# Optimization experiments

Measured on AMD Instinct MI355X. Metric: run time of the kernel, lower is better.

The kernel has to match this reference:

```python
import jax, jax.numpy as jnp
import numpy as np

INPUT_DIM = 1024
MEMORY_DIM = 512
MEMORY_SIZE = 4096
TOPK = 8


def setup_inputs() -> dict:
    key = jax.random.key(0)
    ks = jax.random.split(key, 7)
    query = jax.random.normal(ks[0], (8, 4096, INPUT_DIM), dtype=jnp.float32)
    memory_keys = jax.random.normal(ks[1], (MEMORY_SIZE, MEMORY_DIM), dtype=jnp.float32)
    memory_values = jax.random.normal(ks[2], (MEMORY_SIZE, MEMORY_DIM), dtype=jnp.float32)
    # nn.Linear-style init (uniform +-1/sqrt(fan_in))
    wq = jax.random.uniform(ks[3], (INPUT_DIM, MEMORY_DIM), jnp.float32, -1.0, 1.0) / np.sqrt(INPUT_DIM)
    bq = jax.random.uniform(ks[4], (MEMORY_DIM,), jnp.float32, -1.0, 1.0) / np.sqrt(INPUT_DIM)
    wo = jax.random.uniform(ks[5], (MEMORY_DIM, INPUT_DIM), jnp.float32, -1.0, 1.0) / np.sqrt(MEMORY_DIM)
    bo = jax.random.uniform(ks[6], (INPUT_DIM,), jnp.float32, -1.0, 1.0) / np.sqrt(MEMORY_DIM)
    return {"query": query, "memory_keys": memory_keys, "memory_values": memory_values,
            "wq": wq, "bq": bq, "wo": wo, "bo": bo}


def reference(query, memory_keys, memory_values, wq, bq, wo, bo):
    B, S, D = query.shape
    # Query projection: [B,S,M]
    q = jnp.einsum('bsd,dm->bsm', query, wq) + bq
    # Scores vs memory keys: [B,S,memory_size] (no expand needed)
    scores = jnp.einsum('bsm,km->bsk', q, memory_keys)
    # Top-k selection + softmax over selected scores
    topk_w, topk_idx = jax.lax.top_k(scores, TOPK)           # [B,S,K]
    topk_w = jax.nn.softmax(topk_w, axis=-1)
    # Gather selected memory values: [B,S,K,M]
    top_vals = memory_values[topk_idx]
    mem_out = jnp.einsum('bskm,bsk->bsm', top_vals, topk_w)  # weighted sum
    out = jnp.einsum('bsm,md->bsd', mem_out, wo) + bo
    return out + query
```

## Files before the change

kernel.cpp:

```cpp
#include <hip/hip_runtime.h>
#include <cstdint>

typedef _Float16 f16;
typedef uint32_t u32;
typedef f16 f16x2 __attribute__((ext_vector_type(2)));
typedef f16 f16x8 __attribute__((ext_vector_type(8)));
typedef float f32x4 __attribute__((ext_vector_type(4)));
typedef float f32x16 __attribute__((ext_vector_type(16)));

#define NROWS 32768
#define D_IN 1024
#define M_DIM 512
#define NKEYS 4096
#define KTOP 8

__device__ __forceinline__ u32 umax32(u32 a, u32 b) { return a > b ? a : b; }
__device__ __forceinline__ u32 umin32(u32 a, u32 b) { return a < b ? a : b; }

__device__ __forceinline__ void gload_lds16(const void* src, void* dst) {
  __builtin_amdgcn_global_load_lds(
      (const __attribute__((address_space(1))) uint32_t*)src,
      (__attribute__((address_space(3))) uint32_t*)dst, 16, 0, 0);
}

__global__ void prep_kernel(const float* __restrict__ keys, const float* __restrict__ values,
                            const float* __restrict__ wq, const float* __restrict__ wo,
                            f16* __restrict__ keys_h, f16* __restrict__ values_h,
                            f16* __restrict__ wqT, f16* __restrict__ woT) {
  const int b = blockIdx.x, t = threadIdx.x;
  if (b < 2048) {
    const float* src = (b < 1024) ? keys : values;
    f16* dst = (b < 1024) ? keys_h : values_h;
    const int bb = b & 1023;
    const size_t base = (size_t)bb * 2048 + (size_t)t * 8;
    f32x4 a = *(const f32x4*)(src + base);
    f32x4 c2 = *(const f32x4*)(src + base + 4);
    f16x8 o;
    o[0] = (f16)a[0]; o[1] = (f16)a[1]; o[2] = (f16)a[2]; o[3] = (f16)a[3];
    o[4] = (f16)c2[0]; o[5] = (f16)c2[1]; o[6] = (f16)c2[2]; o[7] = (f16)c2[3];
    *(f16x8*)(dst + base) = o;
  } else if (b < 4096) {
    const int o = (b - 2048) * 256 + t;
    const int m = o >> 10, d = o & 1023;
    wqT[o] = (f16)wq[d * 512 + m];
  } else {
    const int o = (b - 4096) * 256 + t;
    const int od = o >> 9, mm = o & 511;
    woT[o] = (f16)wo[mm * 1024 + od];
  }
}

__global__ __launch_bounds__(256, 2) void qproj_kernel(
    const float* __restrict__ query, const f16* __restrict__ wqT,
    const float* __restrict__ bq, f16* __restrict__ q_out) {
  __shared__ f16 Atile[32 * 1024];
  const int tid = threadIdx.x;
  const int wave = tid >> 6, lane = tid & 63;
  const int g = lane >> 4, c = lane & 15;
  const int rowbase = blockIdx.x * 64 + wave * 16;
  const int row = rowbase + c;

  f16x8 Breg[32];
  {
    const float* qrow = query + (size_t)row * D_IN;
#pragma unroll
    for (int kk = 0; kk < 32; ++kk) {
      f32x4 lo = *(const f32x4*)(qrow + kk * 32 + g * 8);
      f32x4 hi = *(const f32x4*)(qrow + kk * 32 + g * 8 + 4);
      f16x8 v;
      v[0] = (f16)lo[0]; v[1] = (f16)lo[1]; v[2] = (f16)lo[2]; v[3] = (f16)lo[3];
      v[4] = (f16)hi[0]; v[5] = (f16)hi[1]; v[6] = (f16)hi[2]; v[7] = (f16)hi[3];
      Breg[kk] = v;
    }
  }

  for (int mt = 0; mt < 16; ++mt) {
    __syncthreads();
#pragma unroll
    for (int i2 = 0; i2 < 8; ++i2) {
      const int kr = wave * 8 + i2;
#pragma unroll
      for (int hb = 0; hb < 2; ++hb) {
        const u32 slot = (u32)(hb * 1024 + lane * 16);
        const u32 kb = slot ^ (u32)((kr & 7) << 4);
        const char* src = (const char*)(wqT + (size_t)(mt * 32 + kr) * D_IN) + kb;
        gload_lds16(src, (char*)Atile + kr * 2048 + hb * 1024);
      }
    }
    asm volatile("s_waitcnt vmcnt(0)" ::: "memory");
    __syncthreads();

    f32x4 acc0 = {0.f, 0.f, 0.f, 0.f};
    f32x4 acc1 = {0.f, 0.f, 0.f, 0.f};
#pragma unroll
    for (int kk = 0; kk < 32; ++kk) {
      const u32 base = (u32)(kk * 64 + g * 16);
      {
        const int ml = c;
        const u32 off = (u32)(ml * 2048) + (base ^ (u32)((ml & 7) << 4));
        f16x8 a = *(const f16x8*)((const char*)Atile + off);
        acc0 = __builtin_amdgcn_mfma_f32_16x16x32_f16(a, Breg[kk], acc0, 0, 0, 0);
      }
      {
        const int ml = 16 + c;
        const u32 off = (u32)(ml * 2048) + (base ^ (u32)((ml & 7) << 4));
        f16x8 a = *(const f16x8*)((const char*)Atile + off);
        acc1 = __builtin_amdgcn_mfma_f32_16x16x32_f16(a, Breg[kk], acc1, 0, 0, 0);
      }
    }

    f32x4 bq0 = *(const f32x4*)(bq + mt * 32 + g * 4);
    f32x4 bq1 = *(const f32x4*)(bq + mt * 32 + 16 + g * 4);
    f16* qp = q_out + (size_t)row * M_DIM + mt * 32 + g * 4;
    f16x2 p;
    p[0] = (f16)(acc0[0] + bq0[0]); p[1] = (f16)(acc0[1] + bq0[1]); *(f16x2*)(qp + 0) = p;
    p[0] = (f16)(acc0[2] + bq0[2]); p[1] = (f16)(acc0[3] + bq0[3]); *(f16x2*)(qp + 2) = p;
    p[0] = (f16)(acc1[0] + bq1[0]); p[1] = (f16)(acc1[1] + bq1[1]); *(f16x2*)(qp + 16) = p;
    p[0] = (f16)(acc1[2] + bq1[2]); p[1] = (f16)(acc1[3] + bq1[3]); *(f16x2*)(qp + 18) = p;
  }
}

__global__ __launch_bounds__(256, 1) void scores_topk_kernel(
    const f16* __restrict__ q, const f16* __restrict__ keys_h,
    const f16* __restrict__ values_h, f16* __restrict__ mem_out) {
  __shared__ f16 Ktile[2][32 * 512];
  const int tid = threadIdx.x;
  const int wave = tid >> 6, lane = tid & 63;
  const int h = lane >> 5, r32 = lane & 31;
  const int rowbase = blockIdx.x * 128 + wave * 32;
  const int myrow = rowbase + r32;

  f16x8 Breg[32];
  {
    const f16* qr = q + (size_t)myrow * M_DIM;
#pragma unroll
    for (int kk = 0; kk < 32; ++kk)
      Breg[kk] = *(const f16x8*)(qr + kk * 16 + h * 8);
  }

  u32 top[KTOP];
#pragma unroll
  for (int j = 0; j < KTOP; ++j) top[j] = 0u;

  auto stage = [&](int buf, int kt) {
#pragma unroll
    for (int i2 = 0; i2 < 8; ++i2) {
      const int kr = wave * 8 + i2;
      const u32 kb = ((u32)(lane * 16)) ^ ((u32)((kr & 7) << 4));
      const char* src = (const char*)(keys_h + (size_t)(kt * 32 + kr) * M_DIM) + kb;
      gload_lds16(src, (char*)&Ktile[buf][0] + kr * 1024);
    }
  };

  stage(0, 0);
  asm volatile("s_waitcnt vmcnt(0)" ::: "memory");
  __syncthreads();

  for (int kt = 0; kt < 128; ++kt) {
    const int cur = kt & 1;
    if (kt < 127) stage(cur ^ 1, kt + 1);

    f32x16 accA, accB;
#pragma unroll
    for (int i = 0; i < 16; ++i) { accA[i] = 0.f; accB[i] = 0.f; }
    const char* tileb = (const char*)&Ktile[cur][0];
#pragma unroll
    for (int kk = 0; kk < 32; kk += 2) {
      const u32 swz = (u32)((r32 & 7) << 4);
      const u32 offA = (u32)(r32 * 1024) + ((u32)(kk * 32 + h * 16) ^ swz);
      const u32 offB = (u32)(r32 * 1024) + ((u32)((kk + 1) * 32 + h * 16) ^ swz);
      f16x8 aA = *(const f16x8*)(tileb + offA);
      f16x8 aB = *(const f16x8*)(tileb + offB);
      accA = __builtin_amdgcn_mfma_f32_32x32x16_f16(aA, Breg[kk], accA, 0, 0, 0);
      accB = __builtin_amdgcn_mfma_f32_32x32x16_f16(aB, Breg[kk + 1], accB, 0, 0, 0);
    }

#pragma unroll
    for (int i = 0; i < 16; ++i) {
      const float s = accA[i] + accB[i];
      const u32 kidx = (u32)(kt * 32 + (i & 3) + 8 * (i >> 2) + 4 * h);
      const int bi = __float_as_int(s);
      const u32 mono = (u32)bi ^ (u32)((bi >> 31) | 0x80000000);
      u32 x = ((mono + 0x800u) & 0xFFFFF000u) | kidx;
#pragma unroll
      for (int j = 0; j < KTOP; ++j) {
        const u32 nt = umax32(top[j], x);
        x = umin32(top[j], x);
        top[j] = nt;
      }
    }

    asm volatile("s_waitcnt vmcnt(0)" ::: "memory");
    __syncthreads();
  }

  u32 oth[KTOP];
#pragma unroll
  for (int j = 0; j < KTOP; ++j) oth[j] = (u32)__shfl((int)top[j], lane ^ 32);
#pragma unroll
  for (int j = 0; j < KTOP; ++j) {
    u32 x = oth[j];
#pragma unroll
    for (int jj = 0; jj < KTOP; ++jj) {
      const u32 nt = umax32(top[jj], x);
      x = umin32(top[jj], x);
      top[jj] = nt;
    }
  }

  float w[KTOP]; u32 idx[KTOP];
  {
    float s[KTOP];
#pragma unroll
    for (int j = 0; j < KTOP; ++j) {
      const u32 mono = top[j] & 0xFFFFF000u;
      const u32 bits = (mono & 0x80000000u) ? (mono ^ 0x80000000u) : ~mono;
      s[j] = __int_as_float(bits);
      idx[j] = top[j] & 0xFFFu;
    }
    const float m0 = s[0];
    float sum = 0.f;
#pragma unroll
    for (int j = 0; j < KTOP; ++j) { w[j] = __expf(s[j] - m0); sum += w[j]; }
    const float inv = 1.f / sum;
#pragma unroll
    for (int j = 0; j < KTOP; ++j) w[j] *= inv;
  }

  for (int r = 0; r < 32; ++r) {
    float acc2[8];
#pragma unroll
    for (int e = 0; e < 8; ++e) acc2[e] = 0.f;
#pragma unroll
    for (int j = 0; j < KTOP; ++j) {
      const u32 ix = (u32)__shfl((int)idx[j], r);
      const float wj = __shfl(w[j], r);
      const f16x8 v = *(const f16x8*)(values_h + (size_t)ix * M_DIM + lane * 8);
#pragma unroll
      for (int e = 0; e < 8; ++e) acc2[e] += wj * (float)v[e];
    }
    f16x8 o;
#pragma unroll
    for (int e = 0; e < 8; ++e) o[e] = (f16)acc2[e];
    *(f16x8*)(mem_out + (size_t)(rowbase + r) * M_DIM + lane * 8) = o;
  }
}

__global__ __launch_bounds__(256, 2) void outproj_kernel(
    const f16* __restrict__ mem_h, const f16* __restrict__ woT,
    const float* __restrict__ bo, const float* __restrict__ query,
    float* __restrict__ out) {
  __shared__ f16 Atile[32 * 512];
  const int tid = threadIdx.x;
  const int wave = tid >> 6, lane = tid & 63;
  const int g = lane >> 4, c = lane & 15;
  const int rowbase = blockIdx.x * 64 + wave * 16;
  const int row = rowbase + c;

  f16x8 Breg[16];
  {
    const f16* mr = mem_h + (size_t)row * M_DIM;
#pragma unroll
    for (int kk = 0; kk < 16; ++kk)
      Breg[kk] = *(const f16x8*)(mr + kk * 32 + g * 8);
  }

  for (int mt = 0; mt < 32; ++mt) {
    __syncthreads();
#pragma unroll
    for (int i2 = 0; i2 < 8; ++i2) {
      const int kr = wave * 8 + i2;
      const u32 kb = ((u32)(lane * 16)) ^ ((u32)((kr & 7) << 4));
      const char* src = (const char*)(woT + (size_t)(mt * 32 + kr) * M_DIM) + kb;
      gload_lds16(src, (char*)Atile + kr * 1024);
    }
    asm volatile("s_waitcnt vmcnt(0)" ::: "memory");
    __syncthreads();

    f32x4 acc0 = {0.f, 0.f, 0.f, 0.f};
    f32x4 acc1 = {0.f, 0.f, 0.f, 0.f};
#pragma unroll
    for (int kk = 0; kk < 16; ++kk) {
      const u32 base = (u32)(kk * 64 + g * 16);
      {
        const int ml = c;
        const u32 off = (u32)(ml * 1024) + (base ^ (u32)((ml & 7) << 4));
        f16x8 a = *(const f16x8*)((const char*)Atile + off);
        acc0 = __builtin_amdgcn_mfma_f32_16x16x32_f16(a, Breg[kk], acc0, 0, 0, 0);
      }
      {
        const int ml = 16 + c;
        const u32 off = (u32)(ml * 1024) + (base ^ (u32)((ml & 7) << 4));
        f16x8 a = *(const f16x8*)((const char*)Atile + off);
        acc1 = __builtin_amdgcn_mfma_f32_16x16x32_f16(a, Breg[kk], acc1, 0, 0, 0);
      }
    }

    const int od0 = mt * 32 + g * 4;
    f32x4 bo0 = *(const f32x4*)(bo + od0);
    f32x4 bo1 = *(const f32x4*)(bo + od0 + 16);
    const float* qp = query + (size_t)row * D_IN + od0;
    f32x4 q0 = *(const f32x4*)(qp);
    f32x4 q1 = *(const f32x4*)(qp + 16);
    f32x4 o0, o1;
#pragma unroll
    for (int i = 0; i < 4; ++i) {
      o0[i] = acc0[i] + bo0[i] + q0[i];
      o1[i] = acc1[i] + bo1[i] + q1[i];
    }
    float* op = out + (size_t)row * D_IN + od0;
    *(f32x4*)(op) = o0;
    *(f32x4*)(op + 16) = o1;
  }
}

extern "C" void kernel_launch(void* const* d_in, const int* in_sizes, int n_in,
                              void* d_out, int out_size, void* d_ws, size_t ws_size,
                              hipStream_t stream) {
  (void)in_sizes; (void)n_in; (void)out_size;
  const float* query = (const float*)d_in[0];
  const float* mkeys = (const float*)d_in[1];
  const float* mvals = (const float*)d_in[2];
  const float* wq    = (const float*)d_in[3];
  const float* bq    = (const float*)d_in[4];
  const float* wo    = (const float*)d_in[5];
  const float* bo    = (const float*)d_in[6];
  float* out = (float*)d_out;

  char* ws = (char*)d_ws;
  f16* keys_h   = (f16*)(ws);
  f16* values_h = (f16*)(ws + (4u << 20));
  f16* wqT      = (f16*)(ws + (8u << 20));
  f16* woT      = (f16*)(ws + (9u << 20));
  f16* q_h      = (f16*)(ws + (10u << 20));
  f16* mem_h    = (f16*)(ws + (10u << 20) + (size_t)NROWS * M_DIM * 2);
  const size_t need = (10u << 20) + 2ull * (size_t)NROWS * M_DIM * 2;
  if (ws_size < need) return;

  prep_kernel<<<6144, 256, 0, stream>>>(mkeys, mvals, wq, wo, keys_h, values_h, wqT, woT);
  qproj_kernel<<<NROWS / 64, 256, 0, stream>>>(query, wqT, bq, q_h);
  scores_topk_kernel<<<NROWS / 128, 256, 0, stream>>>(q_h, keys_h, values_h, mem_h);
  outproj_kernel<<<NROWS / 64, 256, 0, stream>>>(mem_h, woT, bo, query, out);
}
```

Baseline: 405.7 us.

## Split scores/top-k over key halves, add merge-gather kernel, tile weight transposes

The scores/top-k kernel is split across two key halves, which doubles the grid from 256 to 512 blocks and raises launch bounds to 2 blocks per CU. Each half writes its top-8 candidates to a workspace buffer, and a new merge_gather_kernel merges the two lists, applies softmax and gathers the values. Two interleaved top-k insertion chains shorten the dependency chain, and s_setprio raises wave priority around the MFMA loop. Separately, the weight transposes in prep_kernel now go through LDS tiles so global reads and writes are coalesced, at the cost of an extra kernel launch and a candidate buffer round trip.

```diff
diff --git a/kernel.cpp b/kernel.cpp
--- a/kernel.cpp
+++ b/kernel.cpp
@@ -7,6 +7,7 @@
 typedef f16 f16x8 __attribute__((ext_vector_type(8)));
 typedef float f32x4 __attribute__((ext_vector_type(4)));
 typedef float f32x16 __attribute__((ext_vector_type(16)));
+typedef u32 u32x4 __attribute__((ext_vector_type(4)));
 
 #define NROWS 32768
 #define D_IN 1024
@@ -39,14 +40,37 @@
     o[0] = (f16)a[0]; o[1] = (f16)a[1]; o[2] = (f16)a[2]; o[3] = (f16)a[3];
     o[4] = (f16)c2[0]; o[5] = (f16)c2[1]; o[6] = (f16)c2[2]; o[7] = (f16)c2[3];
     *(f16x8*)(dst + base) = o;
-  } else if (b < 4096) {
-    const int o = (b - 2048) * 256 + t;
-    const int m = o >> 10, d = o & 1023;
-    wqT[o] = (f16)wq[d * 512 + m];
+    return;
+  }
+  __shared__ float lds[64][65];
+  if (b < 2176) {
+    const int tb = b - 2048;
+    const int td = tb >> 3, tm = tb & 7;
+#pragma unroll
+    for (int p = 0; p < 16; ++p) {
+      const int d_loc = p * 4 + (t >> 6), m_loc = t & 63;
+      lds[d_loc][m_loc] = wq[(size_t)(td * 64 + d_loc) * 512 + tm * 64 + m_loc];
+    }
+    __syncthreads();
+#pragma unroll
+    for (int p = 0; p < 16; ++p) {
+      const int m_loc = p * 4 + (t >> 6), d_loc = t & 63;
+      wqT[(size_t)(tm * 64 + m_loc) * 1024 + td * 64 + d_loc] = (f16)lds[d_loc][m_loc];
+    }
   } else {
-    const int o = (b - 4096) * 256 + t;
-    const int od = o >> 9, mm = o & 511;
-    woT[o] = (f16)wo[mm * 1024 + od];
+    const int tb = b - 2176;
+    const int tmm = tb >> 4, tod = tb & 15;
+#pragma unroll
+    for (int p = 0; p < 16; ++p) {
+      const int m_loc = p * 4 + (t >> 6), od_loc = t & 63;
+      lds[m_loc][od_loc] = wo[(size_t)(tmm * 64 + m_loc) * 1024 + tod * 64 + od_loc];
+    }
+    __syncthreads();
+#pragma unroll
+    for (int p = 0; p < 16; ++p) {
+      const int od_loc = p * 4 + (t >> 6), m_loc = t & 63;
+      woT[(size_t)(tod * 64 + od_loc) * 512 + tmm * 64 + m_loc] = (f16)lds[m_loc][od_loc];
+    }
   }
 }
 
@@ -120,15 +144,17 @@
   }
 }
 
-__global__ __launch_bounds__(256, 1) void scores_topk_kernel(
+__global__ __launch_bounds__(256, 2) void scores_topk_kernel(
     const f16* __restrict__ q, const f16* __restrict__ keys_h,
-    const f16* __restrict__ values_h, f16* __restrict__ mem_out) {
+    u32* __restrict__ cand) {
   __shared__ f16 Ktile[2][32 * 512];
   const int tid = threadIdx.x;
   const int wave = tid >> 6, lane = tid & 63;
   const int h = lane >> 5, r32 = lane & 31;
-  const int rowbase = blockIdx.x * 128 + wave * 32;
+  const int rb = blockIdx.x >> 1, half = blockIdx.x & 1;
+  const int rowbase = rb * 128 + wave * 32;
   const int myrow = rowbase + r32;
+  const int keybase = half * 2048;
 
   f16x8 Breg[32];
   {
@@ -138,16 +164,16 @@
       Breg[kk] = *(const f16x8*)(qr + kk * 16 + h * 8);
   }
 
-  u32 top[KTOP];
-#pragma unroll
-  for (int j = 0; j < KTOP; ++j) top[j] = 0u;
+  u32 topE[KTOP], topO[KTOP];
+#pragma unroll
+  for (int j = 0; j < KTOP; ++j) { topE[j] = 0u; topO[j] = 0u; }
 
   auto stage = [&](int buf, int kt) {
 #pragma unroll
     for (int i2 = 0; i2 < 8; ++i2) {
       const int kr = wave * 8 + i2;
       const u32 kb = ((u32)(lane * 16)) ^ ((u32)((kr & 7) << 4));
-      const char* src = (const char*)(keys_h + (size_t)(kt * 32 + kr) * M_DIM) + kb;
+      const char* src = (const char*)(keys_h + (size_t)(keybase + kt * 32 + kr) * M_DIM) + kb;
       gload_lds16(src, (char*)&Ktile[buf][0] + kr * 1024);
     }
   };
@@ -156,14 +182,15 @@
   asm volatile("s_waitcnt vmcnt(0)" ::: "memory");
   __syncthreads();
 
-  for (int kt = 0; kt < 128; ++kt) {
+  for (int kt = 0; kt < 64; ++kt) {
     const int cur = kt & 1;
-    if (kt < 127) stage(cur ^ 1, kt + 1);
+    if (kt < 63) stage(cur ^ 1, kt + 1);
 
     f32x16 accA, accB;
 #pragma unroll
     for (int i = 0; i < 16; ++i) { accA[i] = 0.f; accB[i] = 0.f; }
     const char* tileb = (const char*)&Ktile[cur][0];
+    __builtin_amdgcn_s_setprio(1);
 #pragma unroll
     for (int kk = 0; kk < 32; kk += 2) {
       const u32 swz = (u32)((r32 & 7) << 4);
@@ -174,19 +201,21 @@
       accA = __builtin_amdgcn_mfma_f32_32x32x16_f16(aA, Breg[kk], accA, 0, 0, 0);
       accB = __builtin_amdgcn_mfma_f32_32x32x16_f16(aB, Breg[kk + 1], accB, 0, 0, 0);
     }
+    __builtin_amdgcn_s_setprio(0);
 
 #pragma unroll
     for (int i = 0; i < 16; ++i) {
       const float s = accA[i] + accB[i];
-      const u32 kidx = (u32)(kt * 32 + (i & 3) + 8 * (i >> 2) + 4 * h);
+      const u32 kidx = (u32)(keybase + kt * 32 + (i & 3) + 8 * (i >> 2) + 4 * h);
       const int bi = __float_as_int(s);
       const u32 mono = (u32)bi ^ (u32)((bi >> 31) | 0x80000000);
       u32 x = ((mono + 0x800u) & 0xFFFFF000u) | kidx;
-#pragma unroll
-      for (int j = 0; j < KTOP; ++j) {
-        const u32 nt = umax32(top[j], x);
-        x = umin32(top[j], x);
-        top[j] = nt;
+      if ((i & 1) == 0) {
+#pragma unroll
+        for (int j = 0; j < KTOP; ++j) { const u32 nt = umax32(topE[j], x); x = umin32(topE[j], x); topE[j] = nt; }
+      } else {
+#pragma unroll
+        for (int j = 0; j < KTOP; ++j) { const u32 nt = umax32(topO[j], x); x = umin32(topO[j], x); topO[j] = nt; }
       }
     }
 
@@ -194,18 +223,52 @@
     __syncthreads();
   }
 
+#pragma unroll
+  for (int j = 0; j < KTOP; ++j) {
+    u32 x = topO[j];
+#pragma unroll
+    for (int jj = 0; jj < KTOP; ++jj) { const u32 nt = umax32(topE[jj], x); x = umin32(topE[jj], x); topE[jj] = nt; }
+  }
   u32 oth[KTOP];
 #pragma unroll
-  for (int j = 0; j < KTOP; ++j) oth[j] = (u32)__shfl((int)top[j], lane ^ 32);
+  for (int j = 0; j < KTOP; ++j) oth[j] = (u32)__shfl((int)topE[j], lane ^ 32);
 #pragma unroll
   for (int j = 0; j < KTOP; ++j) {
     u32 x = oth[j];
 #pragma unroll
-    for (int jj = 0; jj < KTOP; ++jj) {
-      const u32 nt = umax32(top[jj], x);
-      x = umin32(top[jj], x);
-      top[jj] = nt;
-    }
+    for (int jj = 0; jj < KTOP; ++jj) { const u32 nt = umax32(topE[jj], x); x = umin32(topE[jj], x); topE[jj] = nt; }
+  }
+
+  if (h == 0) {
+    u32* cp = cand + (size_t)myrow * 16 + half * 8;
+    u32x4 a, b;
+    a.x = topE[0]; a.y = topE[1]; a.z = topE[2]; a.w = topE[3];
+    b.x = topE[4]; b.y = topE[5]; b.z = topE[6]; b.w = topE[7];
+    *(u32x4*)(cp) = a;
+    *(u32x4*)(cp + 4) = b;
+  }
+}
+
+__global__ __launch_bounds__(256, 4) void merge_gather_kernel(
+    const u32* __restrict__ cand, const f16* __restrict__ values_h,
+    f16* __restrict__ mem_out) {
+  const int tid = threadIdx.x;
+  const int wave = tid >> 6, lane = tid & 63;
+  const int rowbase = blockIdx.x * 32 + wave * 8;
+  const int myrow = rowbase + (lane & 7);
+
+  const u32* cp = cand + (size_t)myrow * 16;
+  u32x4 a0 = *(const u32x4*)(cp);
+  u32x4 a1 = *(const u32x4*)(cp + 4);
+  u32x4 b0 = *(const u32x4*)(cp + 8);
+  u32x4 b1 = *(const u32x4*)(cp + 12);
+  u32 top[KTOP] = {a0.x, a0.y, a0.z, a0.w, a1.x, a1.y, a1.z, a1.w};
+  u32 ins[KTOP] = {b0.x, b0.y, b0.z, b0.w, b1.x, b1.y, b1.z, b1.w};
+#pragma unroll
+  for (int j = 0; j < KTOP; ++j) {
+    u32 x = ins[j];
+#pragma unroll
+    for (int jj = 0; jj < KTOP; ++jj) { const u32 nt = umax32(top[jj], x); x = umin32(top[jj], x); top[jj] = nt; }
   }
 
   float w[KTOP]; u32 idx[KTOP];
@@ -227,7 +290,7 @@
     for (int j = 0; j < KTOP; ++j) w[j] *= inv;
   }
 
-  for (int r = 0; r < 32; ++r) {
+  for (int r = 0; r < 8; ++r) {
     float acc2[8];
 #pragma unroll
     for (int e = 0; e < 8; ++e) acc2[e] = 0.f;
@@ -334,11 +397,14 @@
   f16* woT      = (f16*)(ws + (9u << 20));
   f16* q_h      = (f16*)(ws + (10u << 20));
   f16* mem_h    = (f16*)(ws + (10u << 20) + (size_t)NROWS * M_DIM * 2);
-  const size_t need = (10u << 20) + 2ull * (size_t)NROWS * M_DIM * 2;
+  u32* cand     = (u32*)(ws + (10u << 20) + 2ull * (size_t)NROWS * M_DIM * 2);
+  const size_t need = (10u << 20) + 2ull * (size_t)NROWS * M_DIM * 2
+                    + (size_t)NROWS * 16 * 4;
   if (ws_size < need) return;
 
-  prep_kernel<<<6144, 256, 0, stream>>>(mkeys, mvals, wq, wo, keys_h, values_h, wqT, woT);
+  prep_kernel<<<2304, 256, 0, stream>>>(mkeys, mvals, wq, wo, keys_h, values_h, wqT, woT);
   qproj_kernel<<<NROWS / 64, 256, 0, stream>>>(query, wqT, bq, q_h);
-  scores_topk_kernel<<<NROWS / 128, 256, 0, stream>>>(q_h, keys_h, values_h, mem_h);
+  scores_topk_kernel<<<(NROWS / 128) * 2, 256, 0, stream>>>(q_h, keys_h, cand);
+  merge_gather_kernel<<<NROWS / 32, 256, 0, stream>>>(cand, values_h, mem_h);
   outproj_kernel<<<NROWS / 64, 256, 0, stream>>>(mem_h, woT, bo, query, out);
 }
```

New measurement: 367.3 us. 1.1x faster.
